# Kernel tuning notes

Hardware: AMD Instinct MI355X
Metric: run time of the kernel (lower is better)

## Reference

```python
import jax, jax.numpy as jnp
import numpy as np

TAU = 0.6      # init_tau (membrane decay, also scales surrogate h_t)
TAU_O = 0.6    # init_tau_o (output / eligibility kappa filter)
THR = 0.6      # init_thresh (spike threshold)
LR = 0.05      # e-prop grad accumulation factor


def setup_inputs() -> dict:
    key = jax.random.key(0)
    k0, k1, k2, k3, k4 = jax.random.split(key, 5)
    B, T, NI, NH, NO = 64, 100, 700, 512, 20
    # binary spike inputs / one-hot-ish labels (rand -> threshold keeps SNN semantics)
    x = (jax.random.uniform(k0, (B, T, NI)) < 0.3).astype(jnp.float32)
    label = (jax.random.uniform(k1, (B, T, NO)) < 0.5).astype(jnp.float32)
    # kaiming_normal_ then *0.5 for fc1/out; kaiming_normal_ for recurrent
    w_fc1 = jax.random.normal(k2, (NH, NI), jnp.float32) * (0.5 * np.sqrt(2.0 / NI))
    w_rec = jax.random.normal(k3, (NH, NH), jnp.float32) * np.sqrt(2.0 / NH)
    w_out = jax.random.normal(k4, (NO, NH), jnp.float32) * (0.5 * np.sqrt(2.0 / NH))
    return dict(x=x, label=label, training=1, w_fc1=w_fc1, w_rec=w_rec, w_out=w_out)


def reference(x, label, training, w_fc1, w_rec, w_out):
    B, T, NI = x.shape
    NH = w_fc1.shape[0]
    NO = w_out.shape[0]
    dt = x.dtype

    def step(carry, xs):
        (hm, hs, om, os, tin, trec, tout, ein, erec, prev_hs, gf, gr, go) = carry
        xt, lt = xs  # [B,NI], [B,NO]
        # LIF hidden: decay (with reset-by-spike) + input + recurrent
        hidden_input = xt @ w_fc1.T + hs @ w_rec
        hm = TAU * hm * (1.0 - hs) + hidden_input
        hs = (hm >= THR).astype(dt)
        # LIF output
        om = TAU * om * (1.0 - os) + hs @ w_out.T
        os = (om >= THR).astype(dt)
        err = os - lt
        # surrogate derivative (triangle)
        h_t = TAU * jnp.maximum(0.0, 1.0 - jnp.abs((hm - THR) / THR))
        # presynaptic traces (trace_rec uses z_{t-1})
        tin = TAU * tin + xt
        trec = TAU * trec + prev_hs
        # eligibility traces: per-sample outer products, kappa-filtered
        ein = TAU_O * ein + h_t[:, :, None] * tin[:, None, :]    # [B,NH,NI]
        erec = TAU_O * erec + h_t[:, :, None] * trec[:, None, :]  # [B,NH,NH]
        tout = TAU_O * tout + hs
        # learning signal broadcast from output error
        L = err @ w_out  # [B,NH]
        gf = gf + LR * jnp.einsum('br,bri->ri', L, ein)
        gr = gr + LR * jnp.einsum('br,brj->rj', L, erec)
        go = go + LR * jnp.einsum('bo,br->or', err, tout)
        return (hm, hs, om, os, tin, trec, tout, ein, erec, hs, gf, gr, go), os

    z = lambda *s: jnp.zeros(s, dt)
    carry0 = (z(B, NH), z(B, NH), z(B, NO), z(B, NO), z(B, NI), z(B, NH),
              z(B, NH), z(B, NH, NI), z(B, NH, NH), z(B, NH),
              z(NH, NI), z(NH, NH), z(NO, NH))
    xs = (jnp.swapaxes(x, 0, 1), jnp.swapaxes(label, 0, 1))  # time-major
    carryF, outs = jax.lax.scan(step, carry0, xs)
    outputs = jnp.swapaxes(outs, 0, 1)  # [B,T,NO]
    return outputs, carryF[10], carryF[11], carryF[12]
```

## Files before the change

### kernel.cpp

```cpp
#include <hip/hip_runtime.h>
#include <hip/hip_bf16.h>

constexpr int kB  = 64;
constexpr int kT  = 100;
constexpr int kNI = 700;
constexpr int kNH = 512;
constexpr int kNO = 20;
constexpr float TAU   = 0.6f;
constexpr float TAU_O = 0.6f;
constexpr float THR   = 0.6f;
constexpr float LR    = 0.05f;

constexpr size_t BNH = (size_t)kB * kNH;
constexpr size_t BNI = (size_t)kB * kNI;
constexpr size_t BNO = (size_t)kB * kNO;
constexpr int kK   = kT * kB;
constexpr int kKP  = 704;

typedef __attribute__((ext_vector_type(8))) short short8;
typedef __attribute__((ext_vector_type(4))) float f32x4;

constexpr size_t O_XW   = 0;
constexpr size_t O_PGF  = 0;
constexpr size_t O_PGR  = 1572864;
constexpr size_t O_PGO  = 2621440;
constexpr size_t O_HSUR = 3276800;
constexpr size_t O_TIB  = 3276800;
constexpr size_t O_TIN  = 6553600;
constexpr size_t O_HS   = 11033600;
constexpr size_t O_ERR  = 14343168;
constexpr size_t O_WT   = 14471168;
constexpr size_t O_MTB  = 14831616;
constexpr size_t O_TRB  = 16470016;
constexpr size_t O_MSK  = 18108416;
constexpr size_t WS_FLOATS = 18210816;

constexpr size_t OUT_GF = (size_t)kB * kT * kNO;
constexpr size_t OUT_GR = OUT_GF + (size_t)kNH * kNI;
constexpr size_t OUT_GO = OUT_GR + (size_t)kNH * kNH;

__global__ __launch_bounds__(256) void k_prep(const float* __restrict__ w,
                                              const float* __restrict__ x,
                                              float* __restrict__ wT,
                                              float* __restrict__ tin) {
    int bx = blockIdx.x, tid = threadIdx.x;
    if (bx < 352) {
        __shared__ float tile[32][33];
        int i0 = (bx % 22) * 32, r0 = (bx / 22) * 32;
        int tx = tid & 31, ty = tid >> 5;
        #pragma unroll
        for (int k = 0; k < 32; k += 8) {
            int i = i0 + tx;
            tile[ty + k][tx] = (i < kNI) ? w[(size_t)(r0 + ty + k) * kNI + i] : 0.f;
        }
        __syncthreads();
        #pragma unroll
        for (int k = 0; k < 32; k += 8) {
            int i = i0 + ty + k;
            wT[(size_t)i * kNH + r0 + tx] = tile[tx][ty + k];
        }
    } else {
        int idx = (bx - 352) * 256 + tid;
        int b = idx / kNI, i = idx % kNI;
        const float* xp = x + (size_t)b * kT * kNI + i;
        float v = 0.f;
        for (int t = 0; t < kT; t++) {
            v = TAU * v + xp[(size_t)t * kNI];
            tin[(size_t)t * BNI + idx] = v;
        }
    }
}

__global__ __launch_bounds__(256) void k_xw2(const float* __restrict__ x,
                                             const float* __restrict__ wT,
                                             float* __restrict__ XW) {
    int bx = blockIdx.x;
    int mt = bx % 50, nt = bx / 50;
    int m0 = mt * 128, n0 = nt * 128;
    int tid = threadIdx.x, tx = tid & 15, ty = tid >> 4;
    __shared__ float As[128][20];
    __shared__ float Bs[16][128];
    float acc[8][8] = {};
    int arow = tid >> 1, ahalf = tid & 1;
    int bb = (m0 + arow) & 63, tt = (m0 + arow) >> 6;
    const float* ap = x + ((size_t)bb * kT + tt) * kNI;
    for (int k0 = 0; k0 < kKP; k0 += 16) {
        #pragma unroll
        for (int u = 0; u < 2; u++) {
            int k = k0 + ahalf * 8 + u * 4;
            float4 v = (k + 3 < kNI) ? *(const float4*)(ap + k)
                                     : make_float4(0.f, 0.f, 0.f, 0.f);
            *(float4*)&As[arow][ahalf * 8 + u * 4] = v;
        }
        #pragma unroll
        for (int u = 0; u < 2; u++) {
            int f = tid * 2 + u;
            int kk = f >> 5, c4 = f & 31;
            *(float4*)&Bs[kk][c4 * 4] =
                *(const float4*)(wT + (size_t)(k0 + kk) * kNH + n0 + c4 * 4);
        }
        __syncthreads();
        #pragma unroll
        for (int kk = 0; kk < 16; kk++) {
            float av[8];
            #pragma unroll
            for (int i = 0; i < 4; i++) {
                av[i]     = As[ty * 4 + i][kk];
                av[4 + i] = As[64 + ty * 4 + i][kk];
            }
            float4 b0 = *(const float4*)&Bs[kk][tx * 4];
            float4 b1 = *(const float4*)&Bs[kk][64 + tx * 4];
            float bvv[8] = {b0.x, b0.y, b0.z, b0.w, b1.x, b1.y, b1.z, b1.w};
            #pragma unroll
            for (int i = 0; i < 8; i++)
                #pragma unroll
                for (int j = 0; j < 8; j++) acc[i][j] += av[i] * bvv[j];
        }
        __syncthreads();
    }
    #pragma unroll
    for (int i = 0; i < 8; i++) {
        int m = m0 + ((i < 4) ? (ty * 4 + i) : (64 + ty * 4 + i - 4));
        float* dst = XW + (size_t)m * kNH + n0;
        *(float4*)(dst + tx * 4)      = make_float4(acc[i][0], acc[i][1], acc[i][2], acc[i][3]);
        *(float4*)(dst + 64 + tx * 4) = make_float4(acc[i][4], acc[i][5], acc[i][6], acc[i][7]);
    }
}

__global__ __launch_bounds__(832) void k_forward(float* __restrict__ ws,
                                                 const float* __restrict__ label,
                                                 const float* __restrict__ w_rec,
                                                 const float* __restrict__ w_out,
                                                 float* __restrict__ dout,
                                                 unsigned long long* __restrict__ gmask) {
    __shared__ float wout_ld[kNO * kNH];
    __shared__ float partial[8][kNH];
    __shared__ unsigned long long mh[kT * 8];
    __shared__ float errh[kT * kNO];

    int b = blockIdx.x, tid = threadIdx.x;
    int wave = tid >> 6, lane = tid & 63;
    const f32x4* wr4 = (const f32x4*)w_rec;
    for (int e = tid; e < kNO * kNH; e += 832) wout_ld[e] = w_out[e];
    float hm = 0.f, sp_prev = 0.f;
    float om_r[4] = {0.f, 0.f, 0.f, 0.f}, os_r[4] = {0.f, 0.f, 0.f, 0.f};
    int q = wave - 8;
    const int coff = lane * 2;
    __syncthreads();

    for (int t = 0; t < kT; t++) {
        float xw = 0.f;
        if (wave < 8) {
            xw = ws[O_XW + ((size_t)t * 64 + b) * kNH + tid];
            unsigned long long m = (t > 0) ? mh[(t - 1) * 8 + wave] : 0ull;
            const size_t base = (size_t)wave * 64;
            f32x4 s0 = {0.f, 0.f, 0.f, 0.f}, s1 = s0;
            while (m) {
                int j = __builtin_ctzll(m); m &= m - 1;
                const f32x4* r = wr4 + (base + j) * 128 + coff;
                s0 += r[0]; s1 += r[1];
            }
            *(f32x4*)&partial[wave][lane * 8]     = s0;
            *(f32x4*)&partial[wave][lane * 8 + 4] = s1;
        } else if (t > 0) {
            int to = t - 1;
            unsigned long long mk[8];
            #pragma unroll
            for (int k = 0; k < 8; k++) mk[k] = mh[to * 8 + k];
            #pragma unroll
            for (int r = 0; r < 4; r++) {
                int o = q * 4 + r;
                float p = 0.f;
                #pragma unroll
                for (int k = 0; k < 8; k++)
                    if ((mk[k] >> lane) & 1) p += wout_ld[o * kNH + 64 * k + lane];
                #pragma unroll
                for (int off = 32; off >= 1; off >>= 1) p += __shfl_xor(p, off);
                if (lane == 0) {
                    float om_n = TAU * om_r[r] * (1.f - os_r[r]) + p;
                    float os_n = (om_n >= THR) ? 1.f : 0.f;
                    om_r[r] = om_n; os_r[r] = os_n;
                    errh[to * kNO + o] = os_n - label[((size_t)b * kT + to) * kNO + o];
                    dout[((size_t)b * kT + to) * kNO + o] = os_n;
                }
            }
        }
        __syncthreads();
        if (tid < kNH) {
            float rec = ((partial[0][tid] + partial[1][tid]) + (partial[2][tid] + partial[3][tid]))
                      + ((partial[4][tid] + partial[5][tid]) + (partial[6][tid] + partial[7][tid]));
            hm = TAU * hm * (1.f - sp_prev) + (xw + rec);
            bool v = (hm >= THR);
            float sp = v ? 1.f : 0.f;
            sp_prev = sp;
            ws[O_HSUR + (size_t)t * BNH + (size_t)b * kNH + tid] =
                TAU * fmaxf(0.f, 1.f - fabsf(hm - THR) * (1.f / THR));
            unsigned long long bal = __ballot(v);
            if (lane == 0) {
                mh[t * 8 + wave] = bal;
                gmask[((size_t)t * 64 + b) * 8 + wave] = bal;
            }
        }
        __syncthreads();
    }
    if (wave >= 8) {
        int to = kT - 1;
        unsigned long long mk[8];
        #pragma unroll
        for (int k = 0; k < 8; k++) mk[k] = mh[to * 8 + k];
        #pragma unroll
        for (int r = 0; r < 4; r++) {
            int o = q * 4 + r;
            float p = 0.f;
            #pragma unroll
            for (int k = 0; k < 8; k++)
                if ((mk[k] >> lane) & 1) p += wout_ld[o * kNH + 64 * k + lane];
            #pragma unroll
            for (int off = 32; off >= 1; off >>= 1) p += __shfl_xor(p, off);
            if (lane == 0) {
                float om_n = TAU * om_r[r] * (1.f - os_r[r]) + p;
                float os_n = (om_n >= THR) ? 1.f : 0.f;
                errh[to * kNO + o] = os_n - label[((size_t)b * kT + to) * kNO + o];
                dout[((size_t)b * kT + to) * kNO + o] = os_n;
            }
        }
    }
    __syncthreads();
    if (wave == 8 && lane < kNO) {
        float v = 0.f;
        for (int t = kT - 1; t >= 0; t--) {
            v = errh[t * kNO + lane] + TAU_O * v;
            errh[t * kNO + lane] = v;
            ws[O_ERR + (size_t)t * BNO + (size_t)b * kNO + lane] = v;
        }
    }
    __syncthreads();
    if (tid < kNH) {
        float wreg[kNO];
        #pragma unroll
        for (int o = 0; o < kNO; o++) wreg[o] = wout_ld[o * kNH + tid];
        unsigned short* mtb = (unsigned short*)(ws + O_MTB);
        size_t rowoff = (size_t)tid * kK + (size_t)b * 100;
        for (int tq = 0; tq < 25; tq++) {
            unsigned long long w8 = 0;
            #pragma unroll
            for (int u = 0; u < 4; u++) {
                int t = tq * 4 + u;
                float s = 0.f;
                #pragma unroll
                for (int o = 0; o < kNO; o++) s += errh[t * kNO + o] * wreg[o];
                float val = LR * s * ws[O_HSUR + (size_t)t * BNH + (size_t)b * kNH + tid];
                __hip_bfloat16 bv = __float2bfloat16(val);
                w8 |= ((unsigned long long)*(unsigned short*)&bv) << (16 * u);
            }
            *(unsigned long long*)&mtb[rowoff + tq * 4] = w8;
        }
    }
}

__global__ __launch_bounds__(256) void k_post_cast(float* __restrict__ ws,
                                                   const unsigned long long* __restrict__ gmask) {
    int bx = blockIdx.x, tid = threadIdx.x;
    if (bx < 128) {
        size_t idx = (size_t)bx * 256 + tid;
        {
            int b = (int)(idx >> 9), n = (int)(idx & 511);
            int w = n >> 6, bit = n & 63;
            for (int t = 0; t < kT; t++) {
                float cur = (float)((gmask[((size_t)t * 64 + b) * 8 + w] >> bit) & 1ull);
                ws[O_HS + (size_t)(t + 1) * BNH + idx] = cur;
            }
        }
        {
            int n = (int)(idx >> 6), b = (int)(idx & 63);
            int w = n >> 6, bit = n & 63;
            __hip_bfloat16* trb = (__hip_bfloat16*)(ws + O_TRB);
            size_t rowoff = (size_t)n * kK + (size_t)b * 100;
            float v = 0.f, p = 0.f;
            for (int t = 0; t < kT; t++) {
                v = TAU * v + p;
                trb[rowoff + t] = __float2bfloat16(v);
                p = (float)((gmask[((size_t)t * 64 + b) * 8 + w] >> bit) & 1ull);
            }
        }
    } else {
        __shared__ float tile[32][33];
        int v = bx - 128;
        int k0 = (v % 200) * 32, n0 = (v / 200) * 32;
        int tx = tid & 31, ty = tid >> 5;
        const float* src = ws + O_TIN;
        __hip_bfloat16* dst = (__hip_bfloat16*)(ws + O_TIB);
        #pragma unroll
        for (int j = 0; j < 32; j += 8) {
            int kk = k0 + ty + j;
            int bb = kk / 100, tt = kk - bb * 100;
            int n = n0 + tx;
            tile[ty + j][tx] = (n < kNI) ? src[(size_t)tt * BNI + (size_t)bb * kNI + n] : 0.f;
        }
        __syncthreads();
        #pragma unroll
        for (int j = 0; j < 32; j += 8) {
            int n = n0 + ty + j;
            if (n < kNI) dst[(size_t)n * kK + k0 + tx] = __float2bfloat16(tile[tx][ty + j]);
        }
    }
}

__global__ __launch_bounds__(256) void k_grads(float* __restrict__ ws) {
    __shared__ unsigned short As[128 * 72];
    __shared__ unsigned short Bs[128 * 72];
    int bx = blockIdx.x, tid = threadIdx.x;

    if (bx < 160) {
        constexpr int KC = kK / 4, BK = 64, LDT = 72;
        const unsigned short* A = (const unsigned short*)(ws + O_MTB);
        const unsigned short* B;
        float* Cpart;
        int Nrows, ldc, s, mt, nt;
        if (bx < 96) {
            s = bx & 3; mt = (bx >> 2) & 3; nt = bx >> 4;
            B = (const unsigned short*)(ws + O_TIB);
            Cpart = ws + O_PGF; Nrows = kNI; ldc = 768;
        } else {
            int v = bx - 96;
            s = v & 3; mt = (v >> 2) & 3; nt = v >> 4;
            B = (const unsigned short*)(ws + O_TRB);
            Cpart = ws + O_PGR; Nrows = kNH; ldc = kNH;
        }
        int m0 = mt * 128, n0 = nt * 128, k0 = s * KC;
        int wave = tid >> 6, lane = tid & 63;
        int wm = wave & 1, wn = wave >> 1;
        f32x4 acc[4][4];
        #pragma unroll
        for (int i = 0; i < 4; i++)
            #pragma unroll
            for (int j = 0; j < 4; j++) acc[i][j] = (f32x4){0.f, 0.f, 0.f, 0.f};

        for (int kb = 0; kb < KC; kb += BK) {
            int kg = k0 + kb;
            #pragma unroll
            for (int p = 0; p < 4; p++) {
                int f = tid + p * 256;
                int row = f >> 3, seg = f & 7;
                *(short8*)&As[row * LDT + seg * 8] =
                    *(const short8*)&A[(size_t)(m0 + row) * kK + kg + seg * 8];
                short8 bv = {};
                if (n0 + row < Nrows)
                    bv = *(const short8*)&B[(size_t)(n0 + row) * kK + kg + seg * 8];
                *(short8*)&Bs[row * LDT + seg * 8] = bv;
            }
            __syncthreads();
            #pragma unroll
            for (int h = 0; h < 2; h++) {
                int kof = h * 32 + (lane >> 4) * 8;
                short8 af[4], bf[4];
                #pragma unroll
                for (int i = 0; i < 4; i++)
                    af[i] = *(short8*)&As[(wm * 64 + i * 16 + (lane & 15)) * LDT + kof];
                #pragma unroll
                for (int j = 0; j < 4; j++)
                    bf[j] = *(short8*)&Bs[(wn * 64 + j * 16 + (lane & 15)) * LDT + kof];
                #pragma unroll
                for (int i = 0; i < 4; i++)
                    #pragma unroll
                    for (int j = 0; j < 4; j++)
                        acc[i][j] = __builtin_amdgcn_mfma_f32_16x16x32_bf16(af[i], bf[j], acc[i][j], 0, 0, 0);
            }
            __syncthreads();
        }
        float* C = Cpart + (size_t)s * kNH * ldc;
        int rbase = (lane >> 4) * 4, col = lane & 15;
        #pragma unroll
        for (int i = 0; i < 4; i++)
            #pragma unroll
            for (int j = 0; j < 4; j++) {
                int n = n0 + wn * 64 + j * 16 + col;
                #pragma unroll
                for (int r = 0; r < 4; r++) {
                    int m = m0 + wm * 64 + i * 16 + rbase + r;
                    C[(size_t)m * ldc + n] = acc[i][j][r];
                }
            }
    } else {
        float* Asf = (float*)As;
        float* Bsf = (float*)Bs;
        const float* A = ws + O_ERR;
        const float* Bm = ws + O_HS + BNH;
        int v = bx - 160;
        int s = v & 7, nt = v >> 3;
        int n0 = nt * 64, k0 = s * 800;
        int tx = tid & 15, ty = tid >> 4;
        float acc[4][4] = {};
        for (int kb = 0; kb < 800; kb += 16) {
            #pragma unroll
            for (int e = tid; e < 1024; e += 256) {
                int kk = e >> 6, c = e & 63;
                size_t gk = (size_t)(k0 + kb + kk);
                Asf[kk * 64 + c] = (c < kNO) ? A[gk * kNO + c] : 0.f;
                Bsf[kk * 64 + c] = Bm[gk * kNH + n0 + c];
            }
            __syncthreads();
            #pragma unroll
            for (int kk = 0; kk < 16; kk++) {
                float4 av = *(const float4*)&Asf[kk * 64 + ty * 4];
                float4 bv = *(const float4*)&Bsf[kk * 64 + tx * 4];
                float aa[4] = {av.x, av.y, av.z, av.w};
                float bb[4] = {bv.x, bv.y, bv.z, bv.w};
                #pragma unroll
                for (int a = 0; a < 4; a++)
                    #pragma unroll
                    for (int c = 0; c < 4; c++) acc[a][c] += aa[a] * bb[c];
            }
            __syncthreads();
        }
        float* Cs = ws + O_PGO + (size_t)s * kNO * kNH;
        #pragma unroll
        for (int a = 0; a < 4; a++) {
            int m = ty * 4 + a;
            if (m >= kNO) continue;
            #pragma unroll
            for (int c = 0; c < 4; c++)
                Cs[(size_t)m * kNH + n0 + tx * 4 + c] = acc[a][c];
        }
    }
}

__global__ void k_reduce_all(const float* __restrict__ ws, float* __restrict__ dout) {
    int idx = blockIdx.x * 256 + threadIdx.x;
    const int NGF = kNH * kNI, NGR = kNH * kNH, NGO = kNO * kNH;
    float s = 0.f;
    if (idx < NGF) {
        int m = idx / kNI, n = idx - m * kNI;
        size_t src = O_PGF + (size_t)m * 768 + n;
        #pragma unroll
        for (int k = 0; k < 4; k++) s += ws[src + (size_t)k * kNH * 768];
        dout[OUT_GF + idx] = s;
    } else if (idx < NGF + NGR) {
        int j = idx - NGF;
        #pragma unroll
        for (int k = 0; k < 4; k++) s += ws[O_PGR + j + (size_t)k * NGR];
        dout[OUT_GR + j] = s;
    } else if (idx < NGF + NGR + NGO) {
        int j = idx - NGF - NGR;
        #pragma unroll
        for (int k = 0; k < 8; k++) s += ws[O_PGO + (size_t)k * NGO + j];
        dout[OUT_GO + j] = LR * s;
    }
}

extern "C" void kernel_launch(void* const* d_in, const int* in_sizes, int n_in,
                              void* d_out, int out_size, void* d_ws, size_t ws_size,
                              hipStream_t stream) {
    (void)in_sizes; (void)n_in; (void)out_size;
    const float* x     = (const float*)d_in[0];
    const float* label = (const float*)d_in[1];
    const float* w_fc1 = (const float*)d_in[3];
    const float* w_rec = (const float*)d_in[4];
    const float* w_out = (const float*)d_in[5];
    float* out = (float*)d_out;
    float* ws  = (float*)d_ws;

    if (ws_size < WS_FLOATS * sizeof(float)) return;

    unsigned long long* gmask = (unsigned long long*)(ws + O_MSK);

    k_prep<<<527, 256, 0, stream>>>(w_fc1, x, ws + O_WT, ws + O_TIN);
    k_xw2<<<200, 256, 0, stream>>>(x, ws + O_WT, ws + O_XW);

    k_forward<<<kB, 832, 0, stream>>>(ws, label, w_rec, w_out, out, gmask);

    k_post_cast<<<4528, 256, 0, stream>>>(ws, gmask);

    k_grads<<<224, 256, 0, stream>>>(ws);

    k_reduce_all<<<2464, 256, 0, stream>>>(ws, out);
}
```

Before: 659.1 us.

## Eliminate post-cast kernel by fusing its work into neighboring kernels

Removes the k_post_cast launch. Its tin transpose-to-bf16 work now runs as extra blocks of the XW GEMM kernel, and the bf16 recurrent trace is built inside k_forward from the shared spike masks. The go-gradient path now reads spike bits directly from the global mask instead of a materialized float hidden-spike array. This saves one launch and a large float write/read, but adds serial trace work to the forward kernel tail and bit extraction in the grads loads.

```diff
diff --git a/kernel.cpp b/kernel.cpp
--- a/kernel.cpp
+++ b/kernel.cpp
@@ -25,15 +25,14 @@
 constexpr size_t O_PGR  = 1572864;
 constexpr size_t O_PGO  = 2621440;
 constexpr size_t O_HSUR = 3276800;
-constexpr size_t O_TIB  = 3276800;
 constexpr size_t O_TIN  = 6553600;
-constexpr size_t O_HS   = 11033600;
-constexpr size_t O_ERR  = 14343168;
-constexpr size_t O_WT   = 14471168;
-constexpr size_t O_MTB  = 14831616;
-constexpr size_t O_TRB  = 16470016;
-constexpr size_t O_MSK  = 18108416;
-constexpr size_t WS_FLOATS = 18210816;
+constexpr size_t O_ERR  = 11033600;
+constexpr size_t O_WT   = 11161600;
+constexpr size_t O_MTB  = 11522048;
+constexpr size_t O_TRB  = 13160448;
+constexpr size_t O_MSK  = 14798848;
+constexpr size_t O_TIB  = 14901248;
+constexpr size_t WS_FLOATS = 17141248;
 
 constexpr size_t OUT_GF = (size_t)kB * kT * kNO;
 constexpr size_t OUT_GR = OUT_GF + (size_t)kNH * kNI;
@@ -71,59 +70,81 @@
     }
 }
 
-__global__ __launch_bounds__(256) void k_xw2(const float* __restrict__ x,
-                                             const float* __restrict__ wT,
-                                             float* __restrict__ XW) {
-    int bx = blockIdx.x;
-    int mt = bx % 50, nt = bx / 50;
-    int m0 = mt * 128, n0 = nt * 128;
-    int tid = threadIdx.x, tx = tid & 15, ty = tid >> 4;
+__global__ __launch_bounds__(256) void k_xw2c(const float* __restrict__ x,
+                                              const float* __restrict__ wT,
+                                              float* __restrict__ XW,
+                                              const float* __restrict__ tin,
+                                              __hip_bfloat16* __restrict__ tib) {
     __shared__ float As[128][20];
     __shared__ float Bs[16][128];
-    float acc[8][8] = {};
-    int arow = tid >> 1, ahalf = tid & 1;
-    int bb = (m0 + arow) & 63, tt = (m0 + arow) >> 6;
-    const float* ap = x + ((size_t)bb * kT + tt) * kNI;
-    for (int k0 = 0; k0 < kKP; k0 += 16) {
-        #pragma unroll
-        for (int u = 0; u < 2; u++) {
-            int k = k0 + ahalf * 8 + u * 4;
-            float4 v = (k + 3 < kNI) ? *(const float4*)(ap + k)
-                                     : make_float4(0.f, 0.f, 0.f, 0.f);
-            *(float4*)&As[arow][ahalf * 8 + u * 4] = v;
-        }
-        #pragma unroll
-        for (int u = 0; u < 2; u++) {
-            int f = tid * 2 + u;
-            int kk = f >> 5, c4 = f & 31;
-            *(float4*)&Bs[kk][c4 * 4] =
-                *(const float4*)(wT + (size_t)(k0 + kk) * kNH + n0 + c4 * 4);
+    __shared__ float tile[32][33];
+    int bx = blockIdx.x, tid = threadIdx.x;
+    if (bx < 200) {
+        int mt = bx % 50, nt = bx / 50;
+        int m0 = mt * 128, n0 = nt * 128;
+        int tx = tid & 15, ty = tid >> 4;
+        float acc[8][8] = {};
+        int arow = tid >> 1, ahalf = tid & 1;
+        int bb = (m0 + arow) & 63, tt = (m0 + arow) >> 6;
+        const float* ap = x + ((size_t)bb * kT + tt) * kNI;
+        for (int k0 = 0; k0 < kKP; k0 += 16) {
+            #pragma unroll
+            for (int u = 0; u < 2; u++) {
+                int k = k0 + ahalf * 8 + u * 4;
+                float4 v = (k + 3 < kNI) ? *(const float4*)(ap + k)
+                                         : make_float4(0.f, 0.f, 0.f, 0.f);
+                *(float4*)&As[arow][ahalf * 8 + u * 4] = v;
+            }
+            #pragma unroll
+            for (int u = 0; u < 2; u++) {
+                int f = tid * 2 + u;
+                int kk = f >> 5, c4 = f & 31;
+                *(float4*)&Bs[kk][c4 * 4] =
+                    *(const float4*)(wT + (size_t)(k0 + kk) * kNH + n0 + c4 * 4);
+            }
+            __syncthreads();
+            #pragma unroll
+            for (int kk = 0; kk < 16; kk++) {
+                float av[8];
+                #pragma unroll
+                for (int i = 0; i < 4; i++) {
+                    av[i]     = As[ty * 4 + i][kk];
+                    av[4 + i] = As[64 + ty * 4 + i][kk];
+                }
+                float4 b0 = *(const float4*)&Bs[kk][tx * 4];
+                float4 b1 = *(const float4*)&Bs[kk][64 + tx * 4];
+                float bvv[8] = {b0.x, b0.y, b0.z, b0.w, b1.x, b1.y, b1.z, b1.w};
+                #pragma unroll
+                for (int i = 0; i < 8; i++)
+                    #pragma unroll
+                    for (int j = 0; j < 8; j++) acc[i][j] += av[i] * bvv[j];
+            }
+            __syncthreads();
+        }
+        #pragma unroll
+        for (int i = 0; i < 8; i++) {
+            int m = m0 + ((i < 4) ? (ty * 4 + i) : (64 + ty * 4 + i - 4));
+            float* dst = XW + (size_t)m * kNH + n0;
+            *(float4*)(dst + tx * 4)      = make_float4(acc[i][0], acc[i][1], acc[i][2], acc[i][3]);
+            *(float4*)(dst + 64 + tx * 4) = make_float4(acc[i][4], acc[i][5], acc[i][6], acc[i][7]);
+        }
+    } else {
+        int v = bx - 200;
+        int k0 = (v % 200) * 32, n0 = (v / 200) * 32;
+        int tx = tid & 31, ty = tid >> 5;
+        #pragma unroll
+        for (int j = 0; j < 32; j += 8) {
+            int kk = k0 + ty + j;
+            int bb = kk / 100, tt = kk - bb * 100;
+            int n = n0 + tx;
+            tile[ty + j][tx] = (n < kNI) ? tin[(size_t)tt * BNI + (size_t)bb * kNI + n] : 0.f;
         }
         __syncthreads();
         #pragma unroll
-        for (int kk = 0; kk < 16; kk++) {
-            float av[8];
-            #pragma unroll
-            for (int i = 0; i < 4; i++) {
-                av[i]     = As[ty * 4 + i][kk];
-                av[4 + i] = As[64 + ty * 4 + i][kk];
-            }
-            float4 b0 = *(const float4*)&Bs[kk][tx * 4];
-            float4 b1 = *(const float4*)&Bs[kk][64 + tx * 4];
-            float bvv[8] = {b0.x, b0.y, b0.z, b0.w, b1.x, b1.y, b1.z, b1.w};
-            #pragma unroll
-            for (int i = 0; i < 8; i++)
-                #pragma unroll
-                for (int j = 0; j < 8; j++) acc[i][j] += av[i] * bvv[j];
-        }
-        __syncthreads();
-    }
-    #pragma unroll
-    for (int i = 0; i < 8; i++) {
-        int m = m0 + ((i < 4) ? (ty * 4 + i) : (64 + ty * 4 + i - 4));
-        float* dst = XW + (size_t)m * kNH + n0;
-        *(float4*)(dst + tx * 4)      = make_float4(acc[i][0], acc[i][1], acc[i][2], acc[i][3]);
-        *(float4*)(dst + 64 + tx * 4) = make_float4(acc[i][4], acc[i][5], acc[i][6], acc[i][7]);
+        for (int j = 0; j < 32; j += 8) {
+            int n = n0 + ty + j;
+            if (n < kNI) tib[(size_t)n * kK + k0 + tx] = __float2bfloat16(tile[tx][ty + j]);
+        }
     }
 }
 
@@ -225,6 +246,24 @@
             }
         }
     }
+    if (tid < kNH) {
+        unsigned short* trb = (unsigned short*)(ws + O_TRB);
+        size_t rowoff = (size_t)tid * kK + (size_t)b * 100;
+        int w = tid >> 6, bit = tid & 63;
+        float v = 0.f, p = 0.f;
+        for (int tq = 0; tq < 25; tq++) {
+            unsigned long long w8 = 0;
+            #pragma unroll
+            for (int u = 0; u < 4; u++) {
+                int t = tq * 4 + u;
+                v = TAU * v + p;
+                __hip_bfloat16 bv = __float2bfloat16(v);
+                w8 |= ((unsigned long long)*(unsigned short*)&bv) << (16 * u);
+                p = (float)((mh[t * 8 + w] >> bit) & 1ull);
+            }
+            *(unsigned long long*)&trb[rowoff + tq * 4] = w8;
+        }
+    }
     __syncthreads();
     if (wave == 8 && lane < kNO) {
         float v = 0.f;
@@ -254,54 +293,6 @@
                 w8 |= ((unsigned long long)*(unsigned short*)&bv) << (16 * u);
             }
             *(unsigned long long*)&mtb[rowoff + tq * 4] = w8;
-        }
-    }
-}
-
-__global__ __launch_bounds__(256) void k_post_cast(float* __restrict__ ws,
-                                                   const unsigned long long* __restrict__ gmask) {
-    int bx = blockIdx.x, tid = threadIdx.x;
-    if (bx < 128) {
-        size_t idx = (size_t)bx * 256 + tid;
-        {
-            int b = (int)(idx >> 9), n = (int)(idx & 511);
-            int w = n >> 6, bit = n & 63;
-            for (int t = 0; t < kT; t++) {
-                float cur = (float)((gmask[((size_t)t * 64 + b) * 8 + w] >> bit) & 1ull);
-                ws[O_HS + (size_t)(t + 1) * BNH + idx] = cur;
-            }
-        }
-        {
-            int n = (int)(idx >> 6), b = (int)(idx & 63);
-            int w = n >> 6, bit = n & 63;
-            __hip_bfloat16* trb = (__hip_bfloat16*)(ws + O_TRB);
-            size_t rowoff = (size_t)n * kK + (size_t)b * 100;
-            float v = 0.f, p = 0.f;
-            for (int t = 0; t < kT; t++) {
-                v = TAU * v + p;
-                trb[rowoff + t] = __float2bfloat16(v);
-                p = (float)((gmask[((size_t)t * 64 + b) * 8 + w] >> bit) & 1ull);
-            }
-        }
-    } else {
-        __shared__ float tile[32][33];
-        int v = bx - 128;
-        int k0 = (v % 200) * 32, n0 = (v / 200) * 32;
-        int tx = tid & 31, ty = tid >> 5;
-        const float* src = ws + O_TIN;
-        __hip_bfloat16* dst = (__hip_bfloat16*)(ws + O_TIB);
-        #pragma unroll
-        for (int j = 0; j < 32; j += 8) {
-            int kk = k0 + ty + j;
-            int bb = kk / 100, tt = kk - bb * 100;
-            int n = n0 + tx;
-            tile[ty + j][tx] = (n < kNI) ? src[(size_t)tt * BNI + (size_t)bb * kNI + n] : 0.f;
-        }
-        __syncthreads();
-        #pragma unroll
-        for (int j = 0; j < 32; j += 8) {
-            int n = n0 + ty + j;
-            if (n < kNI) dst[(size_t)n * kK + k0 + tx] = __float2bfloat16(tile[tx][ty + j]);
         }
     }
 }
@@ -385,10 +376,11 @@
         float* Asf = (float*)As;
         float* Bsf = (float*)Bs;
         const float* A = ws + O_ERR;
-        const float* Bm = ws + O_HS + BNH;
+        const unsigned long long* gm = (const unsigned long long*)(ws + O_MSK);
         int v = bx - 160;
         int s = v & 7, nt = v >> 3;
         int n0 = nt * 64, k0 = s * 800;
+        int w0 = n0 >> 6;
         int tx = tid & 15, ty = tid >> 4;
         float acc[4][4] = {};
         for (int kb = 0; kb < 800; kb += 16) {
@@ -397,7 +389,7 @@
                 int kk = e >> 6, c = e & 63;
                 size_t gk = (size_t)(k0 + kb + kk);
                 Asf[kk * 64 + c] = (c < kNO) ? A[gk * kNO + c] : 0.f;
-                Bsf[kk * 64 + c] = Bm[gk * kNH + n0 + c];
+                Bsf[kk * 64 + c] = (float)((gm[gk * 8 + w0] >> c) & 1ull);
             }
             __syncthreads();
             #pragma unroll
@@ -462,15 +454,14 @@
 
     if (ws_size < WS_FLOATS * sizeof(float)) return;
 
+    __hip_bfloat16* tib = (__hip_bfloat16*)(ws + O_TIB);
     unsigned long long* gmask = (unsigned long long*)(ws + O_MSK);
 
     k_prep<<<527, 256, 0, stream>>>(w_fc1, x, ws + O_WT, ws + O_TIN);
-    k_xw2<<<200, 256, 0, stream>>>(x, ws + O_WT, ws + O_XW);
+    k_xw2c<<<4600, 256, 0, stream>>>(x, ws + O_WT, ws + O_XW, ws + O_TIN, tib);
 
     k_forward<<<kB, 832, 0, stream>>>(ws, label, w_rec, w_out, out, gmask);
 
-    k_post_cast<<<4528, 256, 0, stream>>>(ws, gmask);
-
     k_grads<<<224, 256, 0, stream>>>(ws);
 
     k_reduce_all<<<2464, 256, 0, stream>>>(ws, out);
```

Result: faster. 637.0 us (-3.4%).
